# Kernel tuning notes

Measured on AMD Instinct MI355X. Metric: run time of the kernel, lower is better.

Reference implementation:

```python
import jax, jax.numpy as jnp
import numpy as np


def setup_inputs() -> dict:
    key = jax.random.key(0)
    ks = jax.random.split(key, 5)
    B, H, W, C = 4, 64, 64, 256
    d = C // 8
    x = jax.random.normal(ks[0], (B, H, W, C), dtype=jnp.float32)
    Wq = jax.random.normal(ks[1], (C, d), dtype=jnp.float32) * (1.0 / np.sqrt(C))
    bq = jnp.zeros((d,), dtype=jnp.float32)
    Wk = jax.random.normal(ks[2], (C, d), dtype=jnp.float32) * (1.0 / np.sqrt(C))
    bk = jnp.zeros((d,), dtype=jnp.float32)
    Wv = jax.random.normal(ks[3], (C, C), dtype=jnp.float32) * (1.0 / np.sqrt(C))
    bv = jnp.zeros((C,), dtype=jnp.float32)
    gamma = jnp.zeros((), dtype=jnp.float32)
    return {"x": x, "Wq": Wq, "bq": bq, "Wk": Wk, "bk": bk, "Wv": Wv, "bv": bv, "gamma": gamma}


def reference(x, Wq, bq, Wk, bk, Wv, bv, gamma):
    B, H, W, C = x.shape
    N = H * W
    xt = x.reshape(B, N, C)  # 1x1 conv == per-pixel dense
    q = xt @ Wq + bq                        # [B, N, d]
    k = xt @ Wk + bk                        # [B, N, d]
    v = xt @ Wv + bv                        # [B, N, C]
    energy = jnp.einsum('bnd,bmd->bnm', q, k)   # Q K^T, [B, N, N]
    attn = jax.nn.softmax(energy, axis=-1)
    # tf: out = matmul(V^T[B,C,N], attn)[B,C,N] then transpose -> out[b,j,c] = sum_i v[b,i,c]*attn[b,i,j]
    out = jnp.einsum('bic,bij->bjc', v, attn)   # [B, N, C]
    out = out.reshape(B, H, W, C)
    return gamma * out + x
```

## Files before the change

### kernel.cpp

```cpp
#include <hip/hip_runtime.h>
#include <hip/hip_bf16.h>


typedef __attribute__((ext_vector_type(4)))  float    f32x4;
typedef __attribute__((ext_vector_type(16))) float    f32x16;
typedef __attribute__((ext_vector_type(8)))  short    bf8;
typedef __attribute__((ext_vector_type(4)))  short    bf4;
typedef __attribute__((ext_vector_type(4)))  unsigned u32x4;

__device__ __forceinline__ short f2bf(float f) {
    unsigned u = __builtin_bit_cast(unsigned, f);
    u += 0x7FFF + ((u >> 16) & 1);
    return (short)(u >> 16);
}
__device__ __forceinline__ float bf2f(short h) {
    unsigned u = ((unsigned)(unsigned short)h) << 16;
    return __builtin_bit_cast(float, u);
}
__device__ __forceinline__ unsigned cvtpk(float lo, float hi) {
    unsigned r;
    asm("v_cvt_pk_bf16_f32 %0, %1, %2" : "=v"(r) : "v"(lo), "v"(hi));
    return r;
}
__device__ __forceinline__ float exp2_fast(float x) {
    float r;
    asm("v_exp_f32 %0, %1" : "=v"(r) : "v"(x));
    return r;
}
__device__ __forceinline__ f32x16 z16() {
    f32x16 v;
#pragma unroll
    for (int i = 0; i < 16; ++i) v[i] = 0.f;
    return v;
}

#define LOG2E 1.44269504088896340736f

__global__ __launch_bounds__(256) void pack_weights(
    const float* __restrict__ Wq, const float* __restrict__ Wk,
    const float* __restrict__ Wv, const float* __restrict__ bq,
    const float* __restrict__ bk, const float* __restrict__ bv,
    short* __restrict__ wallF, float* __restrict__ ball)
{
    int n = blockIdx.x;
    int k = threadIdx.x;
    float w;
    if (n < 32)       w = Wq[k * 32 + n];
    else if (n < 64)  w = Wk[k * 32 + (n - 32)] * LOG2E;
    else              w = Wv[k * 256 + (n - 64)];
    int nf = n >> 4, lcol = n & 15;
    int ks = k >> 5, lg = (k >> 3) & 3, e = k & 7;
    wallF[((size_t)(nf * 8 + ks) * 64 + lg * 16 + lcol) * 8 + e] = f2bf(w);
    if (k == 0) {
        float bias = (n < 32) ? bq[n] : (n < 64) ? bk[n - 32] * LOG2E : bv[n - 64];
        ball[n] = bias;
    }
}

__global__ __launch_bounds__(256) void qkv_gemm(
    const float* __restrict__ x, const short* __restrict__ wallF,
    const float* __restrict__ ball,
    short* __restrict__ qf, short* __restrict__ kf, short* __restrict__ vf)
{
    const int w  = threadIdx.x >> 6;
    const int l  = threadIdx.x & 63;
    const int lr = l & 15;
    const int lg = l >> 4;
    const int m0 = blockIdx.x * 16;

    f32x4 acc[5];
#pragma unroll
    for (int i = 0; i < 5; ++i) acc[i] = (f32x4){0.f, 0.f, 0.f, 0.f};

    const float* xrow = x + (size_t)(m0 + lr) * 256 + lg * 8;
    const short* wwb  = wallF + (size_t)w * 5 * 4096 + l * 8;

#pragma unroll
    for (int ks = 0; ks < 8; ++ks) {
        f32x4 a0 = *(const f32x4*)(xrow + ks * 32);
        f32x4 a1 = *(const f32x4*)(xrow + ks * 32 + 4);
        bf8 af;
#pragma unroll
        for (int t = 0; t < 4; ++t) { af[t] = f2bf(a0[t]); af[t + 4] = f2bf(a1[t]); }
        const short* wb = wwb + (size_t)ks * 512;
#pragma unroll
        for (int nf2 = 0; nf2 < 5; ++nf2) {
            bf8 bfr = *(const bf8*)(wb + (size_t)nf2 * 4096);
            acc[nf2] = __builtin_amdgcn_mfma_f32_16x16x32_bf16(af, bfr, acc[nf2], 0, 0, 0);
        }
    }

    const int b      = m0 >> 12;
    const int i_base = m0 + lg * 4;
#pragma unroll
    for (int nf2 = 0; nf2 < 5; ++nf2) {
        int nf = w * 5 + nf2;
        int n = nf * 16 + lr;
        float bias = ball[n];
        if (nf < 4) {
            int d = n & 31;
            int f = (d >> 4) & 1, sub = (d >> 3) & 1, e = d & 7;
            short* dst = (nf < 2) ? qf : kf;
            size_t base = ((size_t)(b * 128 + (i_base >> 5)) * 2 + f) * 512 + 256 * sub + e;
#pragma unroll
            for (int r = 0; r < 4; ++r) {
                int i31 = (i_base + r) & 31;
                dst[base + (size_t)i31 * 8] = f2bf(acc[nf2][r] + bias);
            }
        } else {
            int c = n - 64;
            bf4 pv;
#pragma unroll
            for (int r = 0; r < 4; ++r) pv[r] = f2bf(acc[nf2][r] + bias);
            size_t addr = (size_t)(b * 256 + (i_base >> 4)) * 4096
                        + (size_t)(c >> 5) * 512
                        + (size_t)((c & 31) + 32 * ((i_base >> 3) & 1)) * 8
                        + (i_base & 7);
            *(bf4*)(vf + addr) = pv;
        }
    }
}

__global__ __launch_bounds__(512) void zsum_kernel(
    const short* __restrict__ qF, const short* __restrict__ kF,
    float* __restrict__ zpart)
{
    const int l = threadIdx.x & 63, w = threadIdx.x >> 6;
    const int b = blockIdx.y;
    const int it0 = blockIdx.x * 2;

    const short* qpa = qF + (size_t)(b * 128 + it0) * 1024 + l * 8;
    bf8 qa0 = *(const bf8*)(qpa);
    bf8 qa1 = *(const bf8*)(qpa + 512);
    bf8 qb0 = *(const bf8*)(qpa + 1024);
    bf8 qb1 = *(const bf8*)(qpa + 1536);

    float zA = 0.f, zB = 0.f;
    const short* kbase = kF + (size_t)b * 131072 + (size_t)w * 16384 + l * 8;
    for (int jt = 0; jt < 16; ++jt) {
        const short* kp = kbase + jt * 1024;
        bf8 kA0 = *(const bf8*)(kp);
        bf8 kA1 = *(const bf8*)(kp + 512);
        f32x16 SA = z16(), SB = z16();
        SA = __builtin_amdgcn_mfma_f32_32x32x16_bf16(kA0, qa0, SA, 0, 0, 0);
        SA = __builtin_amdgcn_mfma_f32_32x32x16_bf16(kA1, qa1, SA, 0, 0, 0);
        SB = __builtin_amdgcn_mfma_f32_32x32x16_bf16(kA0, qb0, SB, 0, 0, 0);
        SB = __builtin_amdgcn_mfma_f32_32x32x16_bf16(kA1, qb1, SB, 0, 0, 0);
#pragma unroll
        for (int r = 0; r < 16; ++r) {
            zA += exp2_fast(fminf(SA[r], 86.f));
            zB += exp2_fast(fminf(SB[r], 86.f));
        }
    }
    zA += __shfl_xor(zA, 32);
    zB += __shfl_xor(zB, 32);
    if (l < 32) {
        zpart[(size_t)w * 16384 + b * 4096 + it0 * 32 + l]      = zA;
        zpart[(size_t)w * 16384 + b * 4096 + it0 * 32 + 32 + l] = zB;
    }
}

__global__ __launch_bounds__(256) void zfinish(
    const float* __restrict__ zpart, float* __restrict__ rz)
{
    int i = blockIdx.x * 256 + threadIdx.x;
    float z = 0.f;
#pragma unroll
    for (int p = 0; p < 8; ++p) z += zpart[p * 16384 + i];
    rz[i] = 1.0f / z;
}

__global__ __launch_bounds__(256) void vscale(
    short* __restrict__ vF, const float* __restrict__ rz)
{
    int t = blockIdx.x * 256 + threadIdx.x;
    size_t base = (size_t)t * 8;
    int b   = (int)(base >> 20);
    int rem = (int)(base & 1048575);
    int it  = rem >> 12;
    int sub = (rem >> 8) & 1;
    int i0  = it * 16 + sub * 8;
    bf8 v = *(bf8*)(vF + base);
    const float* rzp = rz + b * 4096 + i0;
    f32x4 r0 = *(const f32x4*)(rzp);
    f32x4 r1 = *(const f32x4*)(rzp + 4);
#pragma unroll
    for (int e = 0; e < 4; ++e) {
        v[e]     = f2bf(bf2f(v[e])     * r0[e]);
        v[e + 4] = f2bf(bf2f(v[e + 4]) * r1[e]);
    }
    *(bf8*)(vF + base) = v;
}

__global__ __launch_bounds__(512) void attn_out(
    const short* __restrict__ qF, const short* __restrict__ kF,
    const short* __restrict__ vF,
    const float* __restrict__ x, const float* __restrict__ gammaPtr,
    float* __restrict__ out)
{
    __shared__ short Pb[2][4][2][2][64][8];
    __shared__ float red[2][64][128];
    const int l = threadIdx.x & 63, w = threadIdx.x >> 6;
    const int lr = l & 31, hi = l >> 5;
    const int wc = w & 1, isub = w >> 1;

    const int xcd = blockIdx.x & 7, k = blockIdx.x >> 3;
    const int b = xcd >> 1;
    const int jt = (xcd & 1) * 32 + k;
    const int j0 = jt * 64;
    const int c0 = wc * 128;

    const short* kfp = kF + (size_t)(b * 128 + jt * 2 + wc) * 1024 + l * 8;
    bf8 kf0 = *(const bf8*)(kfp);
    bf8 kf1 = *(const bf8*)(kfp + 512);

    f32x16 acc[2][4];
#pragma unroll
    for (int jf = 0; jf < 2; ++jf)
#pragma unroll
        for (int cf = 0; cf < 4; ++cf) acc[jf][cf] = z16();

    const short* qbase = qF + (size_t)b * 131072 + l * 8;
    const short* vbase = vF + (size_t)b * 1048576 + (size_t)(c0 >> 5) * 512 + l * 8;

    short* myP0 = &Pb[0][isub][wc][0][l][0];
    short* myP1 = &Pb[0][isub][wc][1][l][0];
    const size_t PbHalf = sizeof(short) * 4 * 2 * 2 * 64 * 8 / sizeof(short);

    {
        bf8 q0 = *(const bf8*)(qbase + (size_t)isub * 1024);
        bf8 q1 = *(const bf8*)(qbase + (size_t)isub * 1024 + 512);
        f32x16 S = z16();
        S = __builtin_amdgcn_mfma_f32_32x32x16_bf16(q0, kf0, S, 0, 0, 0);
        S = __builtin_amdgcn_mfma_f32_32x32x16_bf16(q1, kf1, S, 0, 0, 0);
        float p[16];
#pragma unroll
        for (int r = 0; r < 16; ++r) p[r] = exp2_fast(fminf(S[r], 86.f));
        unsigned X0 = cvtpk(p[0],  p[1]),  Y0 = cvtpk(p[4],  p[5]);
        unsigned X1 = cvtpk(p[2],  p[3]),  Y1 = cvtpk(p[6],  p[7]);
        unsigned X2 = cvtpk(p[8],  p[9]),  Y2 = cvtpk(p[12], p[13]);
        unsigned X3 = cvtpk(p[10], p[11]), Y3 = cvtpk(p[14], p[15]);
        asm("v_permlane32_swap_b32 %0, %1" : "+v"(X0), "+v"(Y0));
        asm("v_permlane32_swap_b32 %0, %1" : "+v"(X1), "+v"(Y1));
        asm("v_permlane32_swap_b32 %0, %1" : "+v"(X2), "+v"(Y2));
        asm("v_permlane32_swap_b32 %0, %1" : "+v"(X3), "+v"(Y3));
        u32x4 a0w = {X0, X1, Y0, Y1};
        u32x4 a1w = {X2, X3, Y2, Y3};
        *(bf8*)myP0 = __builtin_bit_cast(bf8, a0w);
        *(bf8*)myP1 = __builtin_bit_cast(bf8, a1w);
    }
    bf8 v0[4];
#pragma unroll
    for (int cf = 0; cf < 4; ++cf)
        v0[cf] = *(const bf8*)(vbase + (size_t)isub * 8192 + cf * 512);

    for (int t = 0; t < 32; ++t) {
        __syncthreads();
        const int m = isub + t * 4;
        const short* pb = &Pb[t & 1][isub][0][0][l][0];
        bf8 pa00 = *(const bf8*)(pb);
        bf8 pa01 = *(const bf8*)(pb + 512);
        bf8 pa10 = *(const bf8*)(pb + 1024);
        bf8 pa11 = *(const bf8*)(pb + 1536);

        const short* vp = vbase + (size_t)m * 8192;
        bf8 cv1[4];
#pragma unroll
        for (int cf = 0; cf < 4; ++cf)
            cv1[cf] = *(const bf8*)(vp + 4096 + cf * 512);
        bf8 nv0[4];
#pragma unroll
        for (int cf = 0; cf < 4; ++cf) nv0[cf] = v0[cf];
        if (t < 31) {
            const short* vn = vbase + (size_t)(m + 4) * 8192;
#pragma unroll
            for (int cf = 0; cf < 4; ++cf)
                nv0[cf] = *(const bf8*)(vn + cf * 512);
            const short* qn = qbase + (size_t)(m + 4) * 1024;
            bf8 q0 = *(const bf8*)(qn);
            bf8 q1 = *(const bf8*)(qn + 512);
            f32x16 S = z16();
            S = __builtin_amdgcn_mfma_f32_32x32x16_bf16(q0, kf0, S, 0, 0, 0);
            S = __builtin_amdgcn_mfma_f32_32x32x16_bf16(q1, kf1, S, 0, 0, 0);
            float p[16];
#pragma unroll
            for (int r = 0; r < 16; ++r) p[r] = exp2_fast(fminf(S[r], 86.f));
            unsigned X0 = cvtpk(p[0],  p[1]),  Y0 = cvtpk(p[4],  p[5]);
            unsigned X1 = cvtpk(p[2],  p[3]),  Y1 = cvtpk(p[6],  p[7]);
            unsigned X2 = cvtpk(p[8],  p[9]),  Y2 = cvtpk(p[12], p[13]);
            unsigned X3 = cvtpk(p[10], p[11]), Y3 = cvtpk(p[14], p[15]);
            asm("v_permlane32_swap_b32 %0, %1" : "+v"(X0), "+v"(Y0));
            asm("v_permlane32_swap_b32 %0, %1" : "+v"(X1), "+v"(Y1));
            asm("v_permlane32_swap_b32 %0, %1" : "+v"(X2), "+v"(Y2));
            asm("v_permlane32_swap_b32 %0, %1" : "+v"(X3), "+v"(Y3));
            u32x4 a0w = {X0, X1, Y0, Y1};
            u32x4 a1w = {X2, X3, Y2, Y3};
            short* dst = myP0 + ((t + 1) & 1) * PbHalf;
            *(bf8*)(dst)       = __builtin_bit_cast(bf8, a0w);
            *(bf8*)(dst + 512) = __builtin_bit_cast(bf8, a1w);
        }

        __builtin_amdgcn_s_setprio(1);
#pragma unroll
        for (int cf = 0; cf < 4; ++cf) {
            acc[0][cf] = __builtin_amdgcn_mfma_f32_32x32x16_bf16(pa00, v0[cf],  acc[0][cf], 0, 0, 0);
            acc[0][cf] = __builtin_amdgcn_mfma_f32_32x32x16_bf16(pa01, cv1[cf], acc[0][cf], 0, 0, 0);
            acc[1][cf] = __builtin_amdgcn_mfma_f32_32x32x16_bf16(pa10, v0[cf],  acc[1][cf], 0, 0, 0);
            acc[1][cf] = __builtin_amdgcn_mfma_f32_32x32x16_bf16(pa11, cv1[cf], acc[1][cf], 0, 0, 0);
        }
        __builtin_amdgcn_s_setprio(0);

#pragma unroll
        for (int cf = 0; cf < 4; ++cf) v0[cf] = nv0[cf];
    }

#pragma unroll
    for (int src = 1; src < 4; ++src) {
        if (isub == src) {
#pragma unroll
            for (int jf = 0; jf < 2; ++jf)
#pragma unroll
                for (int cf = 0; cf < 4; ++cf)
#pragma unroll
                    for (int r = 0; r < 16; ++r) {
                        int jrow = (r & 3) + 8 * (r >> 2) + 4 * hi;
                        red[wc][jf * 32 + jrow][cf * 32 + lr] = acc[jf][cf][r];
                    }
        }
        __syncthreads();
        if (isub == 0) {
#pragma unroll
            for (int jf = 0; jf < 2; ++jf)
#pragma unroll
                for (int cf = 0; cf < 4; ++cf)
#pragma unroll
                    for (int r = 0; r < 16; ++r) {
                        int jrow = (r & 3) + 8 * (r >> 2) + 4 * hi;
                        acc[jf][cf][r] += red[wc][jf * 32 + jrow][cf * 32 + lr];
                    }
        }
        __syncthreads();
    }
    if (isub == 0) {
        const float gamma = *gammaPtr;
#pragma unroll
        for (int jf = 0; jf < 2; ++jf)
#pragma unroll
            for (int cf = 0; cf < 4; ++cf)
#pragma unroll
                for (int r = 0; r < 16; ++r) {
                    int jrow = (r & 3) + 8 * (r >> 2) + 4 * hi;
                    int j = j0 + jf * 32 + jrow;
                    size_t idx = (size_t)(b * 4096 + j) * 256 + c0 + cf * 32 + lr;
                    out[idx] = gamma * acc[jf][cf][r] + x[idx];
                }
    }
}

extern "C" void kernel_launch(void* const* d_in, const int* in_sizes, int n_in,
                              void* d_out, int out_size, void* d_ws, size_t ws_size,
                              hipStream_t stream)
{
    const float* x  = (const float*)d_in[0];
    const float* Wq = (const float*)d_in[1];
    const float* bq = (const float*)d_in[2];
    const float* Wk = (const float*)d_in[3];
    const float* bk = (const float*)d_in[4];
    const float* Wv = (const float*)d_in[5];
    const float* bv = (const float*)d_in[6];
    const float* gm = (const float*)d_in[7];
    float* out = (float*)d_out;

    char* wsb = (char*)d_ws;
    short* qf    = (short*)(wsb);
    short* kf    = (short*)(wsb + (1u << 20));
    short* vf    = (short*)(wsb + (2u << 20));
    short* wallF = (short*)(wsb + (10u << 20));
    float* ball  = (float*)(wsb + (10u << 20) + 163840);
    float* zpart = (float*)(wsb + (10u << 20) + 163840 + 1280);
    float* rz    = (float*)(wsb + (10u << 20) + 163840 + 1280 + 524288);

    pack_weights<<<320, 256, 0, stream>>>(Wq, Wk, Wv, bq, bk, bv, wallF, ball);
    qkv_gemm<<<1024, 256, 0, stream>>>(x, wallF, ball, qf, kf, vf);
    zsum_kernel<<<dim3(64, 4), 512, 0, stream>>>(qf, kf, zpart);
    zfinish<<<64, 256, 0, stream>>>(zpart, rz);
    vscale<<<2048, 256, 0, stream>>>(vf, rz);
    attn_out<<<256, 512, 0, stream>>>(qf, kf, vf, x, gm, out);
}
```

Measured before the change: 94.18 us.

## Fold softmax normalizer into exp exponent, drop vscale, retile QKV GEMM

The vscale pass is removed. zfinish now stores -log2(z), and attn_out adds it inside the exponent, so the column normalization is fused into the P computation and V no longer needs an extra read-modify-write pass. The QKV GEMM is retiled so that each wave computes all 20 output fragments for its own 16 rows, using 4x fewer blocks, at the cost of 80 accumulator registers per lane. The __syncthreads in the attention loop is replaced by an explicit lgkmcnt wait plus s_barrier, which avoids waiting on outstanding global loads.

```diff
diff --git a/kernel.cpp b/kernel.cpp
--- a/kernel.cpp
+++ b/kernel.cpp
@@ -12,10 +12,6 @@
     unsigned u = __builtin_bit_cast(unsigned, f);
     u += 0x7FFF + ((u >> 16) & 1);
     return (short)(u >> 16);
-}
-__device__ __forceinline__ float bf2f(short h) {
-    unsigned u = ((unsigned)(unsigned short)h) << 16;
-    return __builtin_bit_cast(float, u);
 }
 __device__ __forceinline__ unsigned cvtpk(float lo, float hi) {
     unsigned r;
@@ -66,14 +62,13 @@
     const int l  = threadIdx.x & 63;
     const int lr = l & 15;
     const int lg = l >> 4;
-    const int m0 = blockIdx.x * 16;
-
-    f32x4 acc[5];
-#pragma unroll
-    for (int i = 0; i < 5; ++i) acc[i] = (f32x4){0.f, 0.f, 0.f, 0.f};
+    const int m0 = blockIdx.x * 64 + w * 16;
+
+    f32x4 acc[20];
+#pragma unroll
+    for (int i = 0; i < 20; ++i) acc[i] = (f32x4){0.f, 0.f, 0.f, 0.f};
 
     const float* xrow = x + (size_t)(m0 + lr) * 256 + lg * 8;
-    const short* wwb  = wallF + (size_t)w * 5 * 4096 + l * 8;
 
 #pragma unroll
     for (int ks = 0; ks < 8; ++ks) {
@@ -82,19 +77,18 @@
         bf8 af;
 #pragma unroll
         for (int t = 0; t < 4; ++t) { af[t] = f2bf(a0[t]); af[t + 4] = f2bf(a1[t]); }
-        const short* wb = wwb + (size_t)ks * 512;
-#pragma unroll
-        for (int nf2 = 0; nf2 < 5; ++nf2) {
-            bf8 bfr = *(const bf8*)(wb + (size_t)nf2 * 4096);
-            acc[nf2] = __builtin_amdgcn_mfma_f32_16x16x32_bf16(af, bfr, acc[nf2], 0, 0, 0);
+        const short* wb = wallF + (size_t)ks * 512 + l * 8;
+#pragma unroll
+        for (int nf = 0; nf < 20; ++nf) {
+            bf8 bfr = *(const bf8*)(wb + (size_t)nf * 4096);
+            acc[nf] = __builtin_amdgcn_mfma_f32_16x16x32_bf16(af, bfr, acc[nf], 0, 0, 0);
         }
     }
 
     const int b      = m0 >> 12;
     const int i_base = m0 + lg * 4;
 #pragma unroll
-    for (int nf2 = 0; nf2 < 5; ++nf2) {
-        int nf = w * 5 + nf2;
+    for (int nf = 0; nf < 20; ++nf) {
         int n = nf * 16 + lr;
         float bias = ball[n];
         if (nf < 4) {
@@ -105,13 +99,13 @@
 #pragma unroll
             for (int r = 0; r < 4; ++r) {
                 int i31 = (i_base + r) & 31;
-                dst[base + (size_t)i31 * 8] = f2bf(acc[nf2][r] + bias);
+                dst[base + (size_t)i31 * 8] = f2bf(acc[nf][r] + bias);
             }
         } else {
             int c = n - 64;
             bf4 pv;
 #pragma unroll
-            for (int r = 0; r < 4; ++r) pv[r] = f2bf(acc[nf2][r] + bias);
+            for (int r = 0; r < 4; ++r) pv[r] = f2bf(acc[nf][r] + bias);
             size_t addr = (size_t)(b * 256 + (i_base >> 4)) * 4096
                         + (size_t)(c >> 5) * 512
                         + (size_t)((c & 31) + 32 * ((i_base >> 3) & 1)) * 8
@@ -161,40 +155,18 @@
 }
 
 __global__ __launch_bounds__(256) void zfinish(
-    const float* __restrict__ zpart, float* __restrict__ rz)
+    const float* __restrict__ zpart, float* __restrict__ lrz)
 {
     int i = blockIdx.x * 256 + threadIdx.x;
     float z = 0.f;
 #pragma unroll
     for (int p = 0; p < 8; ++p) z += zpart[p * 16384 + i];
-    rz[i] = 1.0f / z;
-}
-
-__global__ __launch_bounds__(256) void vscale(
-    short* __restrict__ vF, const float* __restrict__ rz)
-{
-    int t = blockIdx.x * 256 + threadIdx.x;
-    size_t base = (size_t)t * 8;
-    int b   = (int)(base >> 20);
-    int rem = (int)(base & 1048575);
-    int it  = rem >> 12;
-    int sub = (rem >> 8) & 1;
-    int i0  = it * 16 + sub * 8;
-    bf8 v = *(bf8*)(vF + base);
-    const float* rzp = rz + b * 4096 + i0;
-    f32x4 r0 = *(const f32x4*)(rzp);
-    f32x4 r1 = *(const f32x4*)(rzp + 4);
-#pragma unroll
-    for (int e = 0; e < 4; ++e) {
-        v[e]     = f2bf(bf2f(v[e])     * r0[e]);
-        v[e + 4] = f2bf(bf2f(v[e + 4]) * r1[e]);
-    }
-    *(bf8*)(vF + base) = v;
+    lrz[i] = -__log2f(z);
 }
 
 __global__ __launch_bounds__(512) void attn_out(
     const short* __restrict__ qF, const short* __restrict__ kF,
-    const short* __restrict__ vF,
+    const short* __restrict__ vF, const float* __restrict__ lrz,
     const float* __restrict__ x, const float* __restrict__ gammaPtr,
     float* __restrict__ out)
 {
@@ -222,20 +194,30 @@
 
     const short* qbase = qF + (size_t)b * 131072 + l * 8;
     const short* vbase = vF + (size_t)b * 1048576 + (size_t)(c0 >> 5) * 512 + l * 8;
+    const float* lzb   = lrz + b * 4096 + 4 * hi;
 
     short* myP0 = &Pb[0][isub][wc][0][l][0];
     short* myP1 = &Pb[0][isub][wc][1][l][0];
-    const size_t PbHalf = sizeof(short) * 4 * 2 * 2 * 64 * 8 / sizeof(short);
+    const int PbHalf = 4 * 2 * 2 * 64 * 8;
 
     {
         bf8 q0 = *(const bf8*)(qbase + (size_t)isub * 1024);
         bf8 q1 = *(const bf8*)(qbase + (size_t)isub * 1024 + 512);
+        const float* lzt = lzb + isub * 32;
+        f32x4 lz0 = *(const f32x4*)(lzt);
+        f32x4 lz1 = *(const f32x4*)(lzt + 8);
+        f32x4 lz2 = *(const f32x4*)(lzt + 16);
+        f32x4 lz3 = *(const f32x4*)(lzt + 24);
         f32x16 S = z16();
         S = __builtin_amdgcn_mfma_f32_32x32x16_bf16(q0, kf0, S, 0, 0, 0);
         S = __builtin_amdgcn_mfma_f32_32x32x16_bf16(q1, kf1, S, 0, 0, 0);
         float p[16];
 #pragma unroll
-        for (int r = 0; r < 16; ++r) p[r] = exp2_fast(fminf(S[r], 86.f));
+        for (int r = 0; r < 16; ++r) {
+            float lz = (r < 4) ? lz0[r & 3] : (r < 8) ? lz1[r & 3]
+                     : (r < 12) ? lz2[r & 3] : lz3[r & 3];
+            p[r] = exp2_fast(fminf(S[r] + lz, 86.f));
+        }
         unsigned X0 = cvtpk(p[0],  p[1]),  Y0 = cvtpk(p[4],  p[5]);
         unsigned X1 = cvtpk(p[2],  p[3]),  Y1 = cvtpk(p[6],  p[7]);
         unsigned X2 = cvtpk(p[8],  p[9]),  Y2 = cvtpk(p[12], p[13]);
@@ -255,7 +237,10 @@
         v0[cf] = *(const bf8*)(vbase + (size_t)isub * 8192 + cf * 512);
 
     for (int t = 0; t < 32; ++t) {
-        __syncthreads();
+        asm volatile("s_waitcnt lgkmcnt(0)" ::: "memory");
+        __builtin_amdgcn_s_barrier();
+        asm volatile("" ::: "memory");
+
         const int m = isub + t * 4;
         const short* pb = &Pb[t & 1][isub][0][0][l][0];
         bf8 pa00 = *(const bf8*)(pb);
@@ -279,12 +264,21 @@
             const short* qn = qbase + (size_t)(m + 4) * 1024;
             bf8 q0 = *(const bf8*)(qn);
             bf8 q1 = *(const bf8*)(qn + 512);
+            const float* lzt = lzb + (m + 4) * 32;
+            f32x4 lz0 = *(const f32x4*)(lzt);
+            f32x4 lz1 = *(const f32x4*)(lzt + 8);
+            f32x4 lz2 = *(const f32x4*)(lzt + 16);
+            f32x4 lz3 = *(const f32x4*)(lzt + 24);
             f32x16 S = z16();
             S = __builtin_amdgcn_mfma_f32_32x32x16_bf16(q0, kf0, S, 0, 0, 0);
             S = __builtin_amdgcn_mfma_f32_32x32x16_bf16(q1, kf1, S, 0, 0, 0);
             float p[16];
 #pragma unroll
-            for (int r = 0; r < 16; ++r) p[r] = exp2_fast(fminf(S[r], 86.f));
+            for (int r = 0; r < 16; ++r) {
+                float lz = (r < 4) ? lz0[r & 3] : (r < 8) ? lz1[r & 3]
+                         : (r < 12) ? lz2[r & 3] : lz3[r & 3];
+                p[r] = exp2_fast(fminf(S[r] + lz, 86.f));
+            }
             unsigned X0 = cvtpk(p[0],  p[1]),  Y0 = cvtpk(p[4],  p[5]);
             unsigned X1 = cvtpk(p[2],  p[3]),  Y1 = cvtpk(p[6],  p[7]);
             unsigned X2 = cvtpk(p[8],  p[9]),  Y2 = cvtpk(p[12], p[13]);
@@ -378,12 +372,11 @@
     short* wallF = (short*)(wsb + (10u << 20));
     float* ball  = (float*)(wsb + (10u << 20) + 163840);
     float* zpart = (float*)(wsb + (10u << 20) + 163840 + 1280);
-    float* rz    = (float*)(wsb + (10u << 20) + 163840 + 1280 + 524288);
+    float* lrz   = (float*)(wsb + (10u << 20) + 163840 + 1280 + 524288);
 
     pack_weights<<<320, 256, 0, stream>>>(Wq, Wk, Wv, bq, bk, bv, wallF, ball);
-    qkv_gemm<<<1024, 256, 0, stream>>>(x, wallF, ball, qf, kf, vf);
+    qkv_gemm<<<256, 256, 0, stream>>>(x, wallF, ball, qf, kf, vf);
     zsum_kernel<<<dim3(64, 4), 512, 0, stream>>>(qf, kf, zpart);
-    zfinish<<<64, 256, 0, stream>>>(zpart, rz);
-    vscale<<<2048, 256, 0, stream>>>(vf, rz);
-    attn_out<<<256, 512, 0, stream>>>(qf, kf, vf, x, gm, out);
-}
+    zfinish<<<64, 256, 0, stream>>>(zpart, lrz);
+    attn_out<<<256, 512, 0, stream>>>(qf, kf, vf, lrz, x, gm, out);
+}
```

Result: faster. 90.90 us (-3.5%).

## Rework attention kernel to 12 waves with producer/consumer split and retile QKV GEMM

Applied to the files above, without the earlier changes.

The attention-output kernel moves from 8 waves (2 column groups × 4 key subsets) to 12 waves (4 column groups × 3 key subsets). Only two of the four column waves compute the softmax P tiles; all waves consume them for the PV MFMAs, and V loads are no longer prefetched across iterations. The QKV GEMM now has each wave compute all 20 output column fragments for its own 16 rows, with 4× fewer blocks. The goals are more waves to hide latency in attention and better reuse of x in the GEMM. In exchange the change raises register pressure, leaves one of the 43 iterations only partly used, and exposes V load latency inside the loop.

```diff
diff --git a/kernel.cpp b/kernel.cpp
--- a/kernel.cpp
+++ b/kernel.cpp
@@ -66,14 +66,13 @@
     const int l  = threadIdx.x & 63;
     const int lr = l & 15;
     const int lg = l >> 4;
-    const int m0 = blockIdx.x * 16;
-
-    f32x4 acc[5];
-#pragma unroll
-    for (int i = 0; i < 5; ++i) acc[i] = (f32x4){0.f, 0.f, 0.f, 0.f};
+    const int m0 = blockIdx.x * 64 + w * 16;
+
+    f32x4 acc[20];
+#pragma unroll
+    for (int i = 0; i < 20; ++i) acc[i] = (f32x4){0.f, 0.f, 0.f, 0.f};
 
     const float* xrow = x + (size_t)(m0 + lr) * 256 + lg * 8;
-    const short* wwb  = wallF + (size_t)w * 5 * 4096 + l * 8;
 
 #pragma unroll
     for (int ks = 0; ks < 8; ++ks) {
@@ -82,19 +81,18 @@
         bf8 af;
 #pragma unroll
         for (int t = 0; t < 4; ++t) { af[t] = f2bf(a0[t]); af[t + 4] = f2bf(a1[t]); }
-        const short* wb = wwb + (size_t)ks * 512;
-#pragma unroll
-        for (int nf2 = 0; nf2 < 5; ++nf2) {
-            bf8 bfr = *(const bf8*)(wb + (size_t)nf2 * 4096);
-            acc[nf2] = __builtin_amdgcn_mfma_f32_16x16x32_bf16(af, bfr, acc[nf2], 0, 0, 0);
+        const short* wb = wallF + (size_t)ks * 512 + l * 8;
+#pragma unroll
+        for (int nf = 0; nf < 20; ++nf) {
+            bf8 bfr = *(const bf8*)(wb + (size_t)nf * 4096);
+            acc[nf] = __builtin_amdgcn_mfma_f32_16x16x32_bf16(af, bfr, acc[nf], 0, 0, 0);
         }
     }
 
     const int b      = m0 >> 12;
     const int i_base = m0 + lg * 4;
 #pragma unroll
-    for (int nf2 = 0; nf2 < 5; ++nf2) {
-        int nf = w * 5 + nf2;
+    for (int nf = 0; nf < 20; ++nf) {
         int n = nf * 16 + lr;
         float bias = ball[n];
         if (nf < 4) {
@@ -105,13 +103,13 @@
 #pragma unroll
             for (int r = 0; r < 4; ++r) {
                 int i31 = (i_base + r) & 31;
-                dst[base + (size_t)i31 * 8] = f2bf(acc[nf2][r] + bias);
+                dst[base + (size_t)i31 * 8] = f2bf(acc[nf][r] + bias);
             }
         } else {
             int c = n - 64;
             bf4 pv;
 #pragma unroll
-            for (int r = 0; r < 4; ++r) pv[r] = f2bf(acc[nf2][r] + bias);
+            for (int r = 0; r < 4; ++r) pv[r] = f2bf(acc[nf][r] + bias);
             size_t addr = (size_t)(b * 256 + (i_base >> 4)) * 4096
                         + (size_t)(c >> 5) * 512
                         + (size_t)((c & 31) + 32 * ((i_base >> 3) & 1)) * 8
@@ -192,42 +190,42 @@
     *(bf8*)(vF + base) = v;
 }
 
-__global__ __launch_bounds__(512) void attn_out(
+__global__ __launch_bounds__(768, 3) void attn_out(
     const short* __restrict__ qF, const short* __restrict__ kF,
     const short* __restrict__ vF,
     const float* __restrict__ x, const float* __restrict__ gammaPtr,
     float* __restrict__ out)
 {
-    __shared__ short Pb[2][4][2][2][64][8];
-    __shared__ float red[2][64][128];
+    __shared__ short Pb[2][3][2][2][64][8];
+    __shared__ float red[4][64][64];
     const int l = threadIdx.x & 63, w = threadIdx.x >> 6;
     const int lr = l & 31, hi = l >> 5;
-    const int wc = w & 1, isub = w >> 1;
+    const int wc = w & 3, isub = w >> 2;
 
     const int xcd = blockIdx.x & 7, k = blockIdx.x >> 3;
     const int b = xcd >> 1;
     const int jt = (xcd & 1) * 32 + k;
     const int j0 = jt * 64;
-    const int c0 = wc * 128;
-
-    const short* kfp = kF + (size_t)(b * 128 + jt * 2 + wc) * 1024 + l * 8;
+    const int c0 = wc * 64;
+    const bool producer = (wc < 2);
+
+    const short* kfp = kF + (size_t)(b * 128 + jt * 2 + (wc & 1)) * 1024 + l * 8;
     bf8 kf0 = *(const bf8*)(kfp);
     bf8 kf1 = *(const bf8*)(kfp + 512);
 
-    f32x16 acc[2][4];
+    f32x16 acc[2][2];
 #pragma unroll
     for (int jf = 0; jf < 2; ++jf)
 #pragma unroll
-        for (int cf = 0; cf < 4; ++cf) acc[jf][cf] = z16();
+        for (int cf = 0; cf < 2; ++cf) acc[jf][cf] = z16();
 
     const short* qbase = qF + (size_t)b * 131072 + l * 8;
     const short* vbase = vF + (size_t)b * 1048576 + (size_t)(c0 >> 5) * 512 + l * 8;
 
-    short* myP0 = &Pb[0][isub][wc][0][l][0];
-    short* myP1 = &Pb[0][isub][wc][1][l][0];
-    const size_t PbHalf = sizeof(short) * 4 * 2 * 2 * 64 * 8 / sizeof(short);
-
-    {
+    short* myP = &Pb[0][isub][wc & 1][0][l][0];
+    const int PbHalf = 3 * 2 * 2 * 64 * 8;
+
+    if (producer) {
         bf8 q0 = *(const bf8*)(qbase + (size_t)isub * 1024);
         bf8 q1 = *(const bf8*)(qbase + (size_t)isub * 1024 + 512);
         f32x16 S = z16();
@@ -246,37 +244,30 @@
         asm("v_permlane32_swap_b32 %0, %1" : "+v"(X3), "+v"(Y3));
         u32x4 a0w = {X0, X1, Y0, Y1};
         u32x4 a1w = {X2, X3, Y2, Y3};
-        *(bf8*)myP0 = __builtin_bit_cast(bf8, a0w);
-        *(bf8*)myP1 = __builtin_bit_cast(bf8, a1w);
-    }
-    bf8 v0[4];
-#pragma unroll
-    for (int cf = 0; cf < 4; ++cf)
-        v0[cf] = *(const bf8*)(vbase + (size_t)isub * 8192 + cf * 512);
-
-    for (int t = 0; t < 32; ++t) {
-        __syncthreads();
-        const int m = isub + t * 4;
-        const short* pb = &Pb[t & 1][isub][0][0][l][0];
-        bf8 pa00 = *(const bf8*)(pb);
-        bf8 pa01 = *(const bf8*)(pb + 512);
-        bf8 pa10 = *(const bf8*)(pb + 1024);
-        bf8 pa11 = *(const bf8*)(pb + 1536);
-
-        const short* vp = vbase + (size_t)m * 8192;
-        bf8 cv1[4];
-#pragma unroll
-        for (int cf = 0; cf < 4; ++cf)
-            cv1[cf] = *(const bf8*)(vp + 4096 + cf * 512);
-        bf8 nv0[4];
-#pragma unroll
-        for (int cf = 0; cf < 4; ++cf) nv0[cf] = v0[cf];
-        if (t < 31) {
-            const short* vn = vbase + (size_t)(m + 4) * 8192;
-#pragma unroll
-            for (int cf = 0; cf < 4; ++cf)
-                nv0[cf] = *(const bf8*)(vn + cf * 512);
-            const short* qn = qbase + (size_t)(m + 4) * 1024;
+        *(bf8*)(myP)       = __builtin_bit_cast(bf8, a0w);
+        *(bf8*)(myP + 512) = __builtin_bit_cast(bf8, a1w);
+    }
+
+    for (int t = 0; t < 43; ++t) {
+        asm volatile("s_waitcnt lgkmcnt(0)" ::: "memory");
+        __builtin_amdgcn_s_barrier();
+        asm volatile("" ::: "memory");
+
+        const int m = isub + t * 3;
+        const bool work = (m < 128);
+        const int mn = m + 3;
+
+        bf8 pa00, pa01, pa10, pa11;
+        if (work) {
+            const short* pb = &Pb[t & 1][isub][0][0][l][0];
+            pa00 = *(const bf8*)(pb);
+            pa01 = *(const bf8*)(pb + 512);
+            pa10 = *(const bf8*)(pb + 1024);
+            pa11 = *(const bf8*)(pb + 1536);
+        }
+
+        if (producer && mn < 128) {
+            const short* qn = qbase + (size_t)mn * 1024;
             bf8 q0 = *(const bf8*)(qn);
             bf8 q1 = *(const bf8*)(qn + 512);
             f32x16 S = z16();
@@ -295,32 +286,38 @@
             asm("v_permlane32_swap_b32 %0, %1" : "+v"(X3), "+v"(Y3));
             u32x4 a0w = {X0, X1, Y0, Y1};
             u32x4 a1w = {X2, X3, Y2, Y3};
-            short* dst = myP0 + ((t + 1) & 1) * PbHalf;
+            short* dst = myP + ((t + 1) & 1) * PbHalf;
             *(bf8*)(dst)       = __builtin_bit_cast(bf8, a0w);
             *(bf8*)(dst + 512) = __builtin_bit_cast(bf8, a1w);
         }
 
-        __builtin_amdgcn_s_setprio(1);
-#pragma unroll
-        for (int cf = 0; cf < 4; ++cf) {
-            acc[0][cf] = __builtin_amdgcn_mfma_f32_32x32x16_bf16(pa00, v0[cf],  acc[0][cf], 0, 0, 0);
-            acc[0][cf] = __builtin_amdgcn_mfma_f32_32x32x16_bf16(pa01, cv1[cf], acc[0][cf], 0, 0, 0);
-            acc[1][cf] = __builtin_amdgcn_mfma_f32_32x32x16_bf16(pa10, v0[cf],  acc[1][cf], 0, 0, 0);
-            acc[1][cf] = __builtin_amdgcn_mfma_f32_32x32x16_bf16(pa11, cv1[cf], acc[1][cf], 0, 0, 0);
-        }
-        __builtin_amdgcn_s_setprio(0);
-
-#pragma unroll
-        for (int cf = 0; cf < 4; ++cf) v0[cf] = nv0[cf];
-    }
-
-#pragma unroll
-    for (int src = 1; src < 4; ++src) {
+        if (work) {
+            const short* vp = vbase + (size_t)m * 8192;
+            bf8 v00  = *(const bf8*)(vp);
+            bf8 v01  = *(const bf8*)(vp + 512);
+            bf8 cv10 = *(const bf8*)(vp + 4096);
+            bf8 cv11 = *(const bf8*)(vp + 4096 + 512);
+
+            __builtin_amdgcn_s_setprio(1);
+            acc[0][0] = __builtin_amdgcn_mfma_f32_32x32x16_bf16(pa00, v00,  acc[0][0], 0, 0, 0);
+            acc[0][1] = __builtin_amdgcn_mfma_f32_32x32x16_bf16(pa00, v01,  acc[0][1], 0, 0, 0);
+            acc[1][0] = __builtin_amdgcn_mfma_f32_32x32x16_bf16(pa10, v00,  acc[1][0], 0, 0, 0);
+            acc[1][1] = __builtin_amdgcn_mfma_f32_32x32x16_bf16(pa10, v01,  acc[1][1], 0, 0, 0);
+            acc[0][0] = __builtin_amdgcn_mfma_f32_32x32x16_bf16(pa01, cv10, acc[0][0], 0, 0, 0);
+            acc[0][1] = __builtin_amdgcn_mfma_f32_32x32x16_bf16(pa01, cv11, acc[0][1], 0, 0, 0);
+            acc[1][0] = __builtin_amdgcn_mfma_f32_32x32x16_bf16(pa11, cv10, acc[1][0], 0, 0, 0);
+            acc[1][1] = __builtin_amdgcn_mfma_f32_32x32x16_bf16(pa11, cv11, acc[1][1], 0, 0, 0);
+            __builtin_amdgcn_s_setprio(0);
+        }
+    }
+
+#pragma unroll
+    for (int src = 1; src < 3; ++src) {
         if (isub == src) {
 #pragma unroll
             for (int jf = 0; jf < 2; ++jf)
 #pragma unroll
-                for (int cf = 0; cf < 4; ++cf)
+                for (int cf = 0; cf < 2; ++cf)
 #pragma unroll
                     for (int r = 0; r < 16; ++r) {
                         int jrow = (r & 3) + 8 * (r >> 2) + 4 * hi;
@@ -332,7 +329,7 @@
 #pragma unroll
             for (int jf = 0; jf < 2; ++jf)
 #pragma unroll
-                for (int cf = 0; cf < 4; ++cf)
+                for (int cf = 0; cf < 2; ++cf)
 #pragma unroll
                     for (int r = 0; r < 16; ++r) {
                         int jrow = (r & 3) + 8 * (r >> 2) + 4 * hi;
@@ -346,7 +343,7 @@
 #pragma unroll
         for (int jf = 0; jf < 2; ++jf)
 #pragma unroll
-            for (int cf = 0; cf < 4; ++cf)
+            for (int cf = 0; cf < 2; ++cf)
 #pragma unroll
                 for (int r = 0; r < 16; ++r) {
                     int jrow = (r & 3) + 8 * (r >> 2) + 4 * hi;
@@ -381,9 +378,9 @@
     float* rz    = (float*)(wsb + (10u << 20) + 163840 + 1280 + 524288);
 
     pack_weights<<<320, 256, 0, stream>>>(Wq, Wk, Wv, bq, bk, bv, wallF, ball);
-    qkv_gemm<<<1024, 256, 0, stream>>>(x, wallF, ball, qf, kf, vf);
+    qkv_gemm<<<256, 256, 0, stream>>>(x, wallF, ball, qf, kf, vf);
     zsum_kernel<<<dim3(64, 4), 512, 0, stream>>>(qf, kf, zpart);
     zfinish<<<64, 256, 0, stream>>>(zpart, rz);
     vscale<<<2048, 256, 0, stream>>>(vf, rz);
-    attn_out<<<256, 512, 0, stream>>>(qf, kf, vf, x, gm, out);
-}
+    attn_out<<<256, 768, 0, stream>>>(qf, kf, vf, x, gm, out);
+}
```

New measurement: 106.6 us. 13.1% more time.
